# Optimization experiments

Measured on AMD Instinct MI355X. Metric: run time of the kernel, lower is better.

Reference implementation:

```python
import jax, jax.numpy as jnp
import numpy as np

N = 50000      # nodes
E = 800000     # edges (before self-loops)
D = 128        # input_dim
H = 128        # hidden_dim
G = 256        # graphs in batch


def setup_inputs() -> dict:
    key = jax.random.key(0)
    ks = jax.random.split(key, 6)
    x = jax.random.normal(ks[0], (N, D), dtype=jnp.float32)
    edge_index = jax.random.randint(ks[1], (2, E), 0, N, dtype=jnp.int32)
    batch = jnp.sort(jax.random.randint(ks[2], (N,), 0, G, dtype=jnp.int32))
    W1 = jax.random.normal(ks[3], (D, H), dtype=jnp.float32) / np.sqrt(D).astype(np.float32)
    b1 = jnp.zeros((H,), jnp.float32)
    W2 = jax.random.normal(ks[4], (H, H), dtype=jnp.float32) / np.sqrt(H).astype(np.float32)
    b2 = jnp.zeros((H,), jnp.float32)
    alpha = jnp.full((H,), 0.25, jnp.float32)  # PReLU(hidden_dim) init
    return dict(x=x, edge_index=edge_index, batch=batch,
                W1=W1, b1=b1, W2=W2, b2=b2, alpha=alpha)


def _gcn_layer(z, W, b, src, dst, norm):
    # GCNConv: z' = D^{-1/2}(A+I)D^{-1/2} (z W) + b
    zw = z @ W                                            # [N,H] dense GEMM
    agg = jnp.zeros_like(zw).at[dst].add(norm[:, None] * zw[src])  # scatter-add over edges
    return agg + b


def reference(x, edge_index, batch, W1, b1, W2, b2, alpha):
    loop = jnp.arange(N, dtype=edge_index.dtype)
    src = jnp.concatenate([edge_index[0], loop])          # add self-loops
    dst = jnp.concatenate([edge_index[1], loop])
    deg = jnp.zeros((N,), x.dtype).at[dst].add(jnp.float32(1.0))
    dinv = jnp.where(deg > 0, jax.lax.rsqrt(deg), 0.0)
    norm = dinv[src] * dinv[dst]                          # [E+N] edge weights

    zs = []
    z = x
    for (W, b) in ((W1, b1), (W2, b2)):
        z = _gcn_layer(z, W, b, src, dst, norm)
        z = jnp.where(z > 0, z, alpha * z)                # channel-wise PReLU (shared)
        zs.append(z)

    gs = [jax.ops.segment_sum(zi, batch, num_segments=G) for zi in zs]  # global_add_pool
    g = jnp.concatenate(gs, axis=1)                       # [G, num_layers*H]
    return z, g
```

## Files before the change

kernel.cpp:

```cpp
#include <hip/hip_runtime.h>
#include <stdint.h>


#define CAP 96

typedef __attribute__((ext_vector_type(8))) short short8;
typedef __attribute__((ext_vector_type(4))) float f32x4;

__device__ __forceinline__ uint16_t bf16rne(float f) {
    uint32_t u = __float_as_uint(f);
    uint32_t r = (u + 0x7fffu + ((u >> 16) & 1u)) >> 16;
    return (uint16_t)r;
}
__device__ __forceinline__ float bf_lo(uint32_t v) { return __uint_as_float(v << 16); }
__device__ __forceinline__ float bf_hi(uint32_t v) { return __uint_as_float(v & 0xffff0000u); }

__global__ __launch_bounds__(512) void k0(int* __restrict__ cursor, int nbC, int N,
                                          const float* __restrict__ W1,
                                          const float* __restrict__ W2,
                                          uint16_t* __restrict__ Wf1,
                                          uint16_t* __restrict__ Wf2,
                                          float* __restrict__ g_out, int nbZ) {
    int bid = blockIdx.x, t = threadIdx.x;
    if (bid < nbC) {
        int i = bid * 512 + t;
        if (i < N) cursor[i] = 0;
    } else if (bid < nbC + 8) {
        int tid = (bid - nbC) * 512 + t;
        const float* W = (tid & 2048) ? W2 : W1;
        uint16_t* O = (tid & 2048) ? Wf2 : Wf1;
        int q16 = tid & 2047;
        int lane = q16 & 63, n0ks = q16 >> 6;
        int n0 = n0ks >> 2, ks = n0ks & 3;
        int m = lane & 15, quad = lane >> 4;
        int nn = n0 * 16 + m;
        int kkb = ks * 32 + quad * 8;
        uint16_t v[8];
#pragma unroll
        for (int j = 0; j < 8; ++j) v[j] = bf16rne(W[(kkb + j) * 128 + nn]);
        *(short8*)&O[q16 * 8] = *(short8*)v;
    } else {
        int idx = (bid - nbC - 8) * 512 + t;
        ((float4*)g_out)[idx] = make_float4(0.f, 0.f, 0.f, 0.f);
    }
}

__device__ __forceinline__ void gemm_body(const float* Xf, const uint16_t* Xb,
                                          const uint16_t* __restrict__ Wf,
                                          uint16_t* __restrict__ Y, int nrows,
                                          uint16_t* Wl, int bid, int t) {
    int lane = t & 63, w = t >> 6;
    int row0 = bid * 128;
    for (int c = t; c < 2048; c += 512)
        *(short8*)&Wl[c * 8] = *(const short8*)&Wf[c * 8];
    int m = lane & 15, quad = lane >> 4;
    int arow = row0 + w * 16 + m;
    bool rowok = arow < nrows;
    short8 a[4];
    short8 zer = {0, 0, 0, 0, 0, 0, 0, 0};
    if (Xb) {
        const uint16_t* aptr = Xb + (size_t)arow * 128 + quad * 8;
#pragma unroll
        for (int ks = 0; ks < 4; ++ks)
            a[ks] = rowok ? *(const short8*)(aptr + ks * 32) : zer;
    } else {
        const float* ap = Xf + (size_t)arow * 128 + quad * 8;
#pragma unroll
        for (int ks = 0; ks < 4; ++ks) {
            if (rowok) {
                float4 u0 = *(const float4*)(ap + ks * 32);
                float4 u1 = *(const float4*)(ap + ks * 32 + 4);
                uint32_t q[4];
                q[0] = (uint32_t)bf16rne(u0.x) | ((uint32_t)bf16rne(u0.y) << 16);
                q[1] = (uint32_t)bf16rne(u0.z) | ((uint32_t)bf16rne(u0.w) << 16);
                q[2] = (uint32_t)bf16rne(u1.x) | ((uint32_t)bf16rne(u1.y) << 16);
                q[3] = (uint32_t)bf16rne(u1.z) | ((uint32_t)bf16rne(u1.w) << 16);
                a[ks] = *(short8*)q;
            } else a[ks] = zer;
        }
    }
    __syncthreads();

    f32x4 acc[8];
#pragma unroll
    for (int i = 0; i < 8; ++i) acc[i] = (f32x4){0.f, 0.f, 0.f, 0.f};
#pragma unroll
    for (int ks = 0; ks < 4; ++ks)
#pragma unroll
        for (int n0 = 0; n0 < 8; ++n0) {
            short8 b = *(short8*)&Wl[((n0 * 4 + ks) * 64 + lane) * 8];
            acc[n0] = __builtin_amdgcn_mfma_f32_16x16x32_bf16(a[ks], b, acc[n0], 0, 0, 0);
        }
    __syncthreads();

    uint16_t* Ep = Wl;
#pragma unroll
    for (int n0 = 0; n0 < 8; ++n0)
#pragma unroll
        for (int r = 0; r < 4; ++r)
            Ep[(w * 16 + quad * 4 + r) * 136 + n0 * 16 + m] = bf16rne(acc[n0][r]);
    for (int r16 = 0; r16 < 16; ++r16) {
        int row = row0 + w * 16 + r16;
        if (row < nrows) {
            uint32_t v = *(uint32_t*)&Ep[(w * 16 + r16) * 136 + lane * 2];
            ((uint32_t*)Y)[(size_t)row * 64 + lane] = v;
        }
    }
}

__device__ __forceinline__ void fill_body(const int* __restrict__ src, const int* __restrict__ dst,
                                          int* __restrict__ cursor, uint16_t* __restrict__ col,
                                          int E, int fb, int t) {
    int base = fb * 2048 + t;
    int d[4], s[4], p[4];
#pragma unroll
    for (int k = 0; k < 4; ++k) {
        int e = base + k * 512;
        d[k] = (e < E) ? dst[e] : -1;
        s[k] = (e < E) ? src[e] : 0;
    }
#pragma unroll
    for (int k = 0; k < 4; ++k) if (d[k] >= 0) p[k] = atomicAdd(&cursor[d[k]], 1);
#pragma unroll
    for (int k = 0; k < 4; ++k)
        if (d[k] >= 0 && p[k] < CAP) col[(size_t)d[k] * CAP + p[k]] = (uint16_t)s[k];
}

__global__ __launch_bounds__(512, 8) void k5(const float* __restrict__ X,
                                             const uint16_t* __restrict__ Wf,
                                             uint16_t* __restrict__ Y, int nrows, int gemmGrid,
                                             const int* __restrict__ src, const int* __restrict__ dst,
                                             int* __restrict__ cursor, uint16_t* __restrict__ col,
                                             int E, int fillGrid) {
    __shared__ uint16_t Wl[17408];
    int bid = blockIdx.x, t = threadIdx.x;
    int mn = min(gemmGrid, fillGrid), mn2 = 2 * mn;
    int role, idx;
    if (bid < mn2) { role = bid & 1; idx = bid >> 1; }
    else { role = (gemmGrid > fillGrid) ? 0 : 1; idx = bid - mn2 + mn; }
    if (role == 0) gemm_body(X, nullptr, Wf, Y, nrows, Wl, idx, t);
    else fill_body(src, dst, cursor, col, E, idx, t);
}

__global__ __launch_bounds__(512, 8) void gemm2k(const uint16_t* __restrict__ Xb,
                                                 const uint16_t* __restrict__ Wf,
                                                 uint16_t* __restrict__ Y, int nrows) {
    __shared__ uint16_t Wl[17408];
    gemm_body(nullptr, Xb, Wf, Y, nrows, Wl, blockIdx.x, threadIdx.x);
}

__global__ __launch_bounds__(256) void aggp(const uint32_t* __restrict__ zw,
                                            const int* __restrict__ cnt,
                                            const uint16_t* __restrict__ col,
                                            const float* __restrict__ bias,
                                            const float* __restrict__ alpha,
                                            const int* __restrict__ batch,
                                            float* __restrict__ gout, int col_off,
                                            uint32_t* __restrict__ z1b,
                                            float* __restrict__ zoutf,
                                            int mode, int n) {
    __shared__ int gsh[4];
    __shared__ float red[4][128];
    int wv = threadIdx.x >> 6;
    int lane = threadIdx.x & 63;
    int node = blockIdx.x * 4 + wv;
    bool valid = node < n;
    int nc = __builtin_amdgcn_readfirstlane(valid ? node : (n - 1));
    int c = lane * 2;
    int deg = cnt[nc];
    float di = rsqrtf((float)(deg + 1));
    uint32_t sv = zw[(size_t)nc * 64 + lane];
    float ax = di * bf_lo(sv), ay = di * bf_hi(sv);
    float bx = 0.f, by = 0.f;
    int len = min(deg, CAP);
    const uint32_t* cbu = (const uint32_t*)(col + (size_t)nc * CAP);
    uint32_t cc = cbu[lane < 48 ? lane : 0];
    int e = 0;
    for (; e + 7 < len; e += 8) {
        int h = e >> 1;
        uint32_t p0 = (uint32_t)__builtin_amdgcn_readlane((int)cc, h);
        uint32_t p1 = (uint32_t)__builtin_amdgcn_readlane((int)cc, h + 1);
        uint32_t p2 = (uint32_t)__builtin_amdgcn_readlane((int)cc, h + 2);
        uint32_t p3 = (uint32_t)__builtin_amdgcn_readlane((int)cc, h + 3);
        int s0 = (int)(p0 & 0xffffu), s1 = (int)(p0 >> 16);
        int s2 = (int)(p1 & 0xffffu), s3 = (int)(p1 >> 16);
        int s4 = (int)(p2 & 0xffffu), s5 = (int)(p2 >> 16);
        int s6 = (int)(p3 & 0xffffu), s7 = (int)(p3 >> 16);
        uint32_t v0 = zw[(size_t)s0 * 64 + lane];
        uint32_t v1 = zw[(size_t)s1 * 64 + lane];
        uint32_t v2 = zw[(size_t)s2 * 64 + lane];
        uint32_t v3 = zw[(size_t)s3 * 64 + lane];
        uint32_t v4 = zw[(size_t)s4 * 64 + lane];
        uint32_t v5 = zw[(size_t)s5 * 64 + lane];
        uint32_t v6 = zw[(size_t)s6 * 64 + lane];
        uint32_t v7 = zw[(size_t)s7 * 64 + lane];
        float w0 = rsqrtf((float)(cnt[s0] + 1));
        float w1 = rsqrtf((float)(cnt[s1] + 1));
        float w2 = rsqrtf((float)(cnt[s2] + 1));
        float w3 = rsqrtf((float)(cnt[s3] + 1));
        float w4 = rsqrtf((float)(cnt[s4] + 1));
        float w5 = rsqrtf((float)(cnt[s5] + 1));
        float w6 = rsqrtf((float)(cnt[s6] + 1));
        float w7 = rsqrtf((float)(cnt[s7] + 1));
        ax += w0 * bf_lo(v0); ay += w0 * bf_hi(v0);
        bx += w1 * bf_lo(v1); by += w1 * bf_hi(v1);
        ax += w2 * bf_lo(v2); ay += w2 * bf_hi(v2);
        bx += w3 * bf_lo(v3); by += w3 * bf_hi(v3);
        ax += w4 * bf_lo(v4); ay += w4 * bf_hi(v4);
        bx += w5 * bf_lo(v5); by += w5 * bf_hi(v5);
        ax += w6 * bf_lo(v6); ay += w6 * bf_hi(v6);
        bx += w7 * bf_lo(v7); by += w7 * bf_hi(v7);
    }
    for (; e < len; ++e) {
        uint32_t p = (uint32_t)__builtin_amdgcn_readlane((int)cc, e >> 1);
        int s = (e & 1) ? (int)(p >> 16) : (int)(p & 0xffffu);
        float w = rsqrtf((float)(cnt[s] + 1));
        uint32_t v = zw[(size_t)s * 64 + lane];
        ax += w * bf_lo(v); ay += w * bf_hi(v);
    }
    ax += bx; ay += by;
    float zx = di * ax + bias[c];
    float zy = di * ay + bias[c + 1];
    float px = alpha[c], py = alpha[c + 1];
    zx = zx > 0.f ? zx : px * zx;
    zy = zy > 0.f ? zy : py * zy;

    if (valid) {
        if (mode == 0) {
            uint32_t pk = (uint32_t)bf16rne(zx) | ((uint32_t)bf16rne(zy) << 16);
            z1b[(size_t)nc * 64 + lane] = pk;
        } else {
            ((float2*)zoutf)[(size_t)nc * 64 + lane] = make_float2(zx, zy);
        }
    }

    int g = batch[nc];
    float cx = valid ? zx : 0.f, cy = valid ? zy : 0.f;
    if (lane == 0) gsh[wv] = valid ? g : -1 - wv;
    __syncthreads();
    bool uni = (gsh[0] == gsh[1]) && (gsh[1] == gsh[2]) && (gsh[2] == gsh[3]);
    if (uni) {
        red[wv][c] = cx; red[wv][c + 1] = cy;
        __syncthreads();
        if (wv == 0) {
            float sx = red[0][c] + red[1][c] + red[2][c] + red[3][c];
            float sy = red[0][c + 1] + red[1][c + 1] + red[2][c + 1] + red[3][c + 1];
            float* base = &gout[(size_t)g * 256 + col_off];
            atomicAdd(&base[c], sx);
            atomicAdd(&base[c + 1], sy);
        }
    } else {
        __syncthreads();
        if (valid) {
            float* base = &gout[(size_t)g * 256 + col_off];
            atomicAdd(&base[c], cx);
            atomicAdd(&base[c + 1], cy);
        }
    }
}

extern "C" void kernel_launch(void* const* d_in, const int* in_sizes, int n_in,
                              void* d_out, int out_size, void* d_ws, size_t ws_size,
                              hipStream_t stream) {
    const float* x     = (const float*)d_in[0];
    const int*   eidx  = (const int*)d_in[1];
    const int*   batch = (const int*)d_in[2];
    const float* W1    = (const float*)d_in[3];
    const float* b1    = (const float*)d_in[4];
    const float* W2    = (const float*)d_in[5];
    const float* b2    = (const float*)d_in[6];
    const float* alpha = (const float*)d_in[7];

    const int N = in_sizes[2];
    const int E = in_sizes[1] / 2;
    const int G = (out_size - N * 128) / 256;

    const int* src = eidx;
    const int* dst = eidx + E;

    char* ws = (char*)d_ws;
    size_t off = 0;
    auto alloc = [&](size_t bytes) { void* q = ws + off; off = (off + bytes + 255) & ~(size_t)255; return q; };
    int*      cursor = (int*)alloc((size_t)N * 4);
    uint16_t* col    = (uint16_t*)alloc((size_t)N * CAP * 2);
    uint32_t* zw     = (uint32_t*)alloc((size_t)N * 128 * 2);
    uint32_t* z1b    = (uint32_t*)alloc((size_t)N * 128 * 2);
    uint16_t* Wf1    = (uint16_t*)alloc(128 * 128 * 2);
    uint16_t* Wf2    = (uint16_t*)alloc(128 * 128 * 2);

    float* z_out = (float*)d_out;
    float* g_out = (float*)d_out + (size_t)N * 128;

    int nbC      = (N + 511) / 512;
    int nbZ      = (G * 256 / 4 + 511) / 512;
    int fillGrid = (E + 2047) / 2048;
    int gemmGrid = (N + 127) / 128;
    int aggGrid  = (N + 3) / 4;

    k0<<<nbC + 8 + nbZ, 512, 0, stream>>>(cursor, nbC, N, W1, W2, Wf1, Wf2, g_out, nbZ);
    k5<<<gemmGrid + fillGrid, 512, 0, stream>>>(x, Wf1, (uint16_t*)zw, N, gemmGrid,
                                                src, dst, cursor, col, E, fillGrid);
    aggp<<<aggGrid, 256, 0, stream>>>(zw, cursor, col, b1, alpha, batch,
                                      g_out, 0, z1b, nullptr, 0, N);
    gemm2k<<<gemmGrid, 512, 0, stream>>>((const uint16_t*)z1b, Wf2, (uint16_t*)zw, N);
    aggp<<<aggGrid, 256, 0, stream>>>(zw, cursor, col, b2, alpha, batch,
                                      g_out, 128, nullptr, z_out, 1, N);
}
```

Measured before the change: 233.2 us.

## Pad neighbor gather with zero sentinel row, unroll by 16, resize gemm2 and fill blocks

The aggregation loop now walks neighbors 16 at a time. Padding slots point at an extra zeroed sentinel row (index N) with cnt=0, which removes the scalar tail loop and lets more independent gathers be in flight. The second GEMM is launched with 256-thread blocks of 64 rows for more blocks, and each fill block handles 4096 edges instead of 2048. The cost is extra sentinel loads on padded slots, higher register pressure in aggp, and one extra row in the cursor and zw buffers.

Measured after the change: 244.9 us. +5.0%, slower.

```diff
diff --git a/kernel.cpp b/kernel.cpp
--- a/kernel.cpp
+++ b/kernel.cpp
@@ -20,11 +20,13 @@
                                           const float* __restrict__ W2,
                                           uint16_t* __restrict__ Wf1,
                                           uint16_t* __restrict__ Wf2,
-                                          float* __restrict__ g_out, int nbZ) {
+                                          float* __restrict__ g_out, int nbZ,
+                                          uint32_t* __restrict__ zw) {
     int bid = blockIdx.x, t = threadIdx.x;
     if (bid < nbC) {
         int i = bid * 512 + t;
-        if (i < N) cursor[i] = 0;
+        if (i <= N) cursor[i] = 0;
+        if (bid == 0 && t < 64) zw[(size_t)N * 64 + t] = 0u;
     } else if (bid < nbC + 8) {
         int tid = (bid - nbC) * 512 + t;
         const float* W = (tid & 2048) ? W2 : W1;
@@ -45,13 +47,14 @@
     }
 }
 
+template <int NW>
 __device__ __forceinline__ void gemm_body(const float* Xf, const uint16_t* Xb,
                                           const uint16_t* __restrict__ Wf,
                                           uint16_t* __restrict__ Y, int nrows,
                                           uint16_t* Wl, int bid, int t) {
     int lane = t & 63, w = t >> 6;
-    int row0 = bid * 128;
-    for (int c = t; c < 2048; c += 512)
+    int row0 = bid * (NW * 16);
+    for (int c = t; c < 2048; c += NW * 64)
         *(short8*)&Wl[c * 8] = *(const short8*)&Wf[c * 8];
     int m = lane & 15, quad = lane >> 4;
     int arow = row0 + w * 16 + m;
@@ -111,18 +114,18 @@
 __device__ __forceinline__ void fill_body(const int* __restrict__ src, const int* __restrict__ dst,
                                           int* __restrict__ cursor, uint16_t* __restrict__ col,
                                           int E, int fb, int t) {
-    int base = fb * 2048 + t;
-    int d[4], s[4], p[4];
-#pragma unroll
-    for (int k = 0; k < 4; ++k) {
+    int base = fb * 4096 + t;
+    int d[8], s[8], p[8];
+#pragma unroll
+    for (int k = 0; k < 8; ++k) {
         int e = base + k * 512;
         d[k] = (e < E) ? dst[e] : -1;
         s[k] = (e < E) ? src[e] : 0;
     }
 #pragma unroll
-    for (int k = 0; k < 4; ++k) if (d[k] >= 0) p[k] = atomicAdd(&cursor[d[k]], 1);
-#pragma unroll
-    for (int k = 0; k < 4; ++k)
+    for (int k = 0; k < 8; ++k) if (d[k] >= 0) p[k] = atomicAdd(&cursor[d[k]], 1);
+#pragma unroll
+    for (int k = 0; k < 8; ++k)
         if (d[k] >= 0 && p[k] < CAP) col[(size_t)d[k] * CAP + p[k]] = (uint16_t)s[k];
 }
 
@@ -138,15 +141,15 @@
     int role, idx;
     if (bid < mn2) { role = bid & 1; idx = bid >> 1; }
     else { role = (gemmGrid > fillGrid) ? 0 : 1; idx = bid - mn2 + mn; }
-    if (role == 0) gemm_body(X, nullptr, Wf, Y, nrows, Wl, idx, t);
+    if (role == 0) gemm_body<8>(X, nullptr, Wf, Y, nrows, Wl, idx, t);
     else fill_body(src, dst, cursor, col, E, idx, t);
 }
 
-__global__ __launch_bounds__(512, 8) void gemm2k(const uint16_t* __restrict__ Xb,
+__global__ __launch_bounds__(256, 4) void gemm2k(const uint16_t* __restrict__ Xb,
                                                  const uint16_t* __restrict__ Wf,
                                                  uint16_t* __restrict__ Y, int nrows) {
     __shared__ uint16_t Wl[17408];
-    gemm_body(nullptr, Xb, Wf, Y, nrows, Wl, blockIdx.x, threadIdx.x);
+    gemm_body<4>(nullptr, Xb, Wf, Y, nrows, Wl, blockIdx.x, threadIdx.x);
 }
 
 __global__ __launch_bounds__(256) void aggp(const uint32_t* __restrict__ zw,
@@ -173,19 +176,99 @@
     float ax = di * bf_lo(sv), ay = di * bf_hi(sv);
     float bx = 0.f, by = 0.f;
     int len = min(deg, CAP);
+    int len8 = (len + 7) & ~7;
     const uint32_t* cbu = (const uint32_t*)(col + (size_t)nc * CAP);
     uint32_t cc = cbu[lane < 48 ? lane : 0];
     int e = 0;
-    for (; e + 7 < len; e += 8) {
+    for (; e + 16 <= len8; e += 16) {
         int h = e >> 1;
-        uint32_t p0 = (uint32_t)__builtin_amdgcn_readlane((int)cc, h);
-        uint32_t p1 = (uint32_t)__builtin_amdgcn_readlane((int)cc, h + 1);
-        uint32_t p2 = (uint32_t)__builtin_amdgcn_readlane((int)cc, h + 2);
-        uint32_t p3 = (uint32_t)__builtin_amdgcn_readlane((int)cc, h + 3);
-        int s0 = (int)(p0 & 0xffffu), s1 = (int)(p0 >> 16);
-        int s2 = (int)(p1 & 0xffffu), s3 = (int)(p1 >> 16);
-        int s4 = (int)(p2 & 0xffffu), s5 = (int)(p2 >> 16);
-        int s6 = (int)(p3 & 0xffffu), s7 = (int)(p3 >> 16);
+        uint32_t q0 = (uint32_t)__builtin_amdgcn_readlane((int)cc, h);
+        uint32_t q1 = (uint32_t)__builtin_amdgcn_readlane((int)cc, h + 1);
+        uint32_t q2 = (uint32_t)__builtin_amdgcn_readlane((int)cc, h + 2);
+        uint32_t q3 = (uint32_t)__builtin_amdgcn_readlane((int)cc, h + 3);
+        uint32_t q4 = (uint32_t)__builtin_amdgcn_readlane((int)cc, h + 4);
+        uint32_t q5 = (uint32_t)__builtin_amdgcn_readlane((int)cc, h + 5);
+        uint32_t q6 = (uint32_t)__builtin_amdgcn_readlane((int)cc, h + 6);
+        uint32_t q7 = (uint32_t)__builtin_amdgcn_readlane((int)cc, h + 7);
+        int s0  = (e +  0 < len) ? (int)(q0 & 0xffffu) : n;
+        int s1  = (e +  1 < len) ? (int)(q0 >> 16)     : n;
+        int s2  = (e +  2 < len) ? (int)(q1 & 0xffffu) : n;
+        int s3  = (e +  3 < len) ? (int)(q1 >> 16)     : n;
+        int s4  = (e +  4 < len) ? (int)(q2 & 0xffffu) : n;
+        int s5  = (e +  5 < len) ? (int)(q2 >> 16)     : n;
+        int s6  = (e +  6 < len) ? (int)(q3 & 0xffffu) : n;
+        int s7  = (e +  7 < len) ? (int)(q3 >> 16)     : n;
+        int s8  = (e +  8 < len) ? (int)(q4 & 0xffffu) : n;
+        int s9  = (e +  9 < len) ? (int)(q4 >> 16)     : n;
+        int s10 = (e + 10 < len) ? (int)(q5 & 0xffffu) : n;
+        int s11 = (e + 11 < len) ? (int)(q5 >> 16)     : n;
+        int s12 = (e + 12 < len) ? (int)(q6 & 0xffffu) : n;
+        int s13 = (e + 13 < len) ? (int)(q6 >> 16)     : n;
+        int s14 = (e + 14 < len) ? (int)(q7 & 0xffffu) : n;
+        int s15 = (e + 15 < len) ? (int)(q7 >> 16)     : n;
+        uint32_t v0  = zw[(size_t)s0  * 64 + lane];
+        uint32_t v1  = zw[(size_t)s1  * 64 + lane];
+        uint32_t v2  = zw[(size_t)s2  * 64 + lane];
+        uint32_t v3  = zw[(size_t)s3  * 64 + lane];
+        uint32_t v4  = zw[(size_t)s4  * 64 + lane];
+        uint32_t v5  = zw[(size_t)s5  * 64 + lane];
+        uint32_t v6  = zw[(size_t)s6  * 64 + lane];
+        uint32_t v7  = zw[(size_t)s7  * 64 + lane];
+        uint32_t v8  = zw[(size_t)s8  * 64 + lane];
+        uint32_t v9  = zw[(size_t)s9  * 64 + lane];
+        uint32_t v10 = zw[(size_t)s10 * 64 + lane];
+        uint32_t v11 = zw[(size_t)s11 * 64 + lane];
+        uint32_t v12 = zw[(size_t)s12 * 64 + lane];
+        uint32_t v13 = zw[(size_t)s13 * 64 + lane];
+        uint32_t v14 = zw[(size_t)s14 * 64 + lane];
+        uint32_t v15 = zw[(size_t)s15 * 64 + lane];
+        float w0  = rsqrtf((float)(cnt[s0]  + 1));
+        float w1  = rsqrtf((float)(cnt[s1]  + 1));
+        float w2  = rsqrtf((float)(cnt[s2]  + 1));
+        float w3  = rsqrtf((float)(cnt[s3]  + 1));
+        float w4  = rsqrtf((float)(cnt[s4]  + 1));
+        float w5  = rsqrtf((float)(cnt[s5]  + 1));
+        float w6  = rsqrtf((float)(cnt[s6]  + 1));
+        float w7  = rsqrtf((float)(cnt[s7]  + 1));
+        float w8  = rsqrtf((float)(cnt[s8]  + 1));
+        float w9  = rsqrtf((float)(cnt[s9]  + 1));
+        float w10 = rsqrtf((float)(cnt[s10] + 1));
+        float w11 = rsqrtf((float)(cnt[s11] + 1));
+        float w12 = rsqrtf((float)(cnt[s12] + 1));
+        float w13 = rsqrtf((float)(cnt[s13] + 1));
+        float w14 = rsqrtf((float)(cnt[s14] + 1));
+        float w15 = rsqrtf((float)(cnt[s15] + 1));
+        ax += w0  * bf_lo(v0);  ay += w0  * bf_hi(v0);
+        bx += w1  * bf_lo(v1);  by += w1  * bf_hi(v1);
+        ax += w2  * bf_lo(v2);  ay += w2  * bf_hi(v2);
+        bx += w3  * bf_lo(v3);  by += w3  * bf_hi(v3);
+        ax += w4  * bf_lo(v4);  ay += w4  * bf_hi(v4);
+        bx += w5  * bf_lo(v5);  by += w5  * bf_hi(v5);
+        ax += w6  * bf_lo(v6);  ay += w6  * bf_hi(v6);
+        bx += w7  * bf_lo(v7);  by += w7  * bf_hi(v7);
+        ax += w8  * bf_lo(v8);  ay += w8  * bf_hi(v8);
+        bx += w9  * bf_lo(v9);  by += w9  * bf_hi(v9);
+        ax += w10 * bf_lo(v10); ay += w10 * bf_hi(v10);
+        bx += w11 * bf_lo(v11); by += w11 * bf_hi(v11);
+        ax += w12 * bf_lo(v12); ay += w12 * bf_hi(v12);
+        bx += w13 * bf_lo(v13); by += w13 * bf_hi(v13);
+        ax += w14 * bf_lo(v14); ay += w14 * bf_hi(v14);
+        bx += w15 * bf_lo(v15); by += w15 * bf_hi(v15);
+    }
+    if (e < len8) {
+        int h = e >> 1;
+        uint32_t q0 = (uint32_t)__builtin_amdgcn_readlane((int)cc, h);
+        uint32_t q1 = (uint32_t)__builtin_amdgcn_readlane((int)cc, h + 1);
+        uint32_t q2 = (uint32_t)__builtin_amdgcn_readlane((int)cc, h + 2);
+        uint32_t q3 = (uint32_t)__builtin_amdgcn_readlane((int)cc, h + 3);
+        int s0 = (e + 0 < len) ? (int)(q0 & 0xffffu) : n;
+        int s1 = (e + 1 < len) ? (int)(q0 >> 16)     : n;
+        int s2 = (e + 2 < len) ? (int)(q1 & 0xffffu) : n;
+        int s3 = (e + 3 < len) ? (int)(q1 >> 16)     : n;
+        int s4 = (e + 4 < len) ? (int)(q2 & 0xffffu) : n;
+        int s5 = (e + 5 < len) ? (int)(q2 >> 16)     : n;
+        int s6 = (e + 6 < len) ? (int)(q3 & 0xffffu) : n;
+        int s7 = (e + 7 < len) ? (int)(q3 >> 16)     : n;
         uint32_t v0 = zw[(size_t)s0 * 64 + lane];
         uint32_t v1 = zw[(size_t)s1 * 64 + lane];
         uint32_t v2 = zw[(size_t)s2 * 64 + lane];
@@ -211,13 +294,6 @@
         ax += w6 * bf_lo(v6); ay += w6 * bf_hi(v6);
         bx += w7 * bf_lo(v7); by += w7 * bf_hi(v7);
     }
-    for (; e < len; ++e) {
-        uint32_t p = (uint32_t)__builtin_amdgcn_readlane((int)cc, e >> 1);
-        int s = (e & 1) ? (int)(p >> 16) : (int)(p & 0xffffu);
-        float w = rsqrtf((float)(cnt[s] + 1));
-        uint32_t v = zw[(size_t)s * 64 + lane];
-        ax += w * bf_lo(v); ay += w * bf_hi(v);
-    }
     ax += bx; ay += by;
     float zx = di * ax + bias[c];
     float zy = di * ay + bias[c + 1];
@@ -281,9 +357,9 @@
     char* ws = (char*)d_ws;
     size_t off = 0;
     auto alloc = [&](size_t bytes) { void* q = ws + off; off = (off + bytes + 255) & ~(size_t)255; return q; };
-    int*      cursor = (int*)alloc((size_t)N * 4);
+    int*      cursor = (int*)alloc((size_t)(N + 1) * 4);
     uint16_t* col    = (uint16_t*)alloc((size_t)N * CAP * 2);
-    uint32_t* zw     = (uint32_t*)alloc((size_t)N * 128 * 2);
+    uint32_t* zw     = (uint32_t*)alloc((size_t)(N + 1) * 128 * 2);
     uint32_t* z1b    = (uint32_t*)alloc((size_t)N * 128 * 2);
     uint16_t* Wf1    = (uint16_t*)alloc(128 * 128 * 2);
     uint16_t* Wf2    = (uint16_t*)alloc(128 * 128 * 2);
@@ -291,18 +367,19 @@
     float* z_out = (float*)d_out;
     float* g_out = (float*)d_out + (size_t)N * 128;
 
-    int nbC      = (N + 511) / 512;
+    int nbC      = (N + 512) / 512;
     int nbZ      = (G * 256 / 4 + 511) / 512;
-    int fillGrid = (E + 2047) / 2048;
+    int fillGrid = (E + 4095) / 4096;
     int gemmGrid = (N + 127) / 128;
+    int gemm2Grid = (N + 63) / 64;
     int aggGrid  = (N + 3) / 4;
 
-    k0<<<nbC + 8 + nbZ, 512, 0, stream>>>(cursor, nbC, N, W1, W2, Wf1, Wf2, g_out, nbZ);
+    k0<<<nbC + 8 + nbZ, 512, 0, stream>>>(cursor, nbC, N, W1, W2, Wf1, Wf2, g_out, nbZ, zw);
     k5<<<gemmGrid + fillGrid, 512, 0, stream>>>(x, Wf1, (uint16_t*)zw, N, gemmGrid,
                                                 src, dst, cursor, col, E, fillGrid);
     aggp<<<aggGrid, 256, 0, stream>>>(zw, cursor, col, b1, alpha, batch,
                                       g_out, 0, z1b, nullptr, 0, N);
-    gemm2k<<<gemmGrid, 512, 0, stream>>>((const uint16_t*)z1b, Wf2, (uint16_t*)zw, N);
+    gemm2k<<<gemm2Grid, 256, 0, stream>>>((const uint16_t*)z1b, Wf2, (uint16_t*)zw, N);
     aggp<<<aggGrid, 256, 0, stream>>>(zw, cursor, col, b2, alpha, batch,
                                       g_out, 128, nullptr, z_out, 1, N);
 }
```

## Prescale layer-2 GEMM rows by source degree norm and pad gathers to 16-wide

Applied to the files above, without the earlier changes.

The second GEMM now multiplies each output row by rsqrt(deg+1), so the layer-2 aggregation no longer has to gather cnt[s] and compute rsqrt per edge. The aggregation loop is also restructured to issue 16 independent gathers per iteration. Out-of-range slots are padded to a dummy zero row at index N, which removes the scalar tail loop. This adds an extra zero row to zw and cursor. It also applies bf16 rounding after the degree scaling in layer 2, which changes numerics slightly.

Result: faster. 228.3 us (-2.1%).

```diff
diff --git a/kernel.cpp b/kernel.cpp
--- a/kernel.cpp
+++ b/kernel.cpp
@@ -20,11 +20,13 @@
                                           const float* __restrict__ W2,
                                           uint16_t* __restrict__ Wf1,
                                           uint16_t* __restrict__ Wf2,
-                                          float* __restrict__ g_out, int nbZ) {
+                                          float* __restrict__ g_out, int nbZ,
+                                          uint32_t* __restrict__ zw) {
     int bid = blockIdx.x, t = threadIdx.x;
     if (bid < nbC) {
         int i = bid * 512 + t;
-        if (i < N) cursor[i] = 0;
+        if (i <= N) cursor[i] = 0;
+        if (bid == 0 && t < 64) zw[(size_t)N * 64 + t] = 0u;
     } else if (bid < nbC + 8) {
         int tid = (bid - nbC) * 512 + t;
         const float* W = (tid & 2048) ? W2 : W1;
@@ -48,6 +50,7 @@
 __device__ __forceinline__ void gemm_body(const float* Xf, const uint16_t* Xb,
                                           const uint16_t* __restrict__ Wf,
                                           uint16_t* __restrict__ Y, int nrows,
+                                          const int* __restrict__ cnt,
                                           uint16_t* Wl, int bid, int t) {
     int lane = t & 63, w = t >> 6;
     int row0 = bid * 128;
@@ -93,12 +96,22 @@
         }
     __syncthreads();
 
+    float dsc[4] = {1.f, 1.f, 1.f, 1.f};
+    if (cnt) {
+#pragma unroll
+        for (int r = 0; r < 4; ++r) {
+            int gr = row0 + w * 16 + quad * 4 + r;
+            int d = (gr < nrows) ? cnt[gr] : 0;
+            dsc[r] = rsqrtf((float)(d + 1));
+        }
+    }
+
     uint16_t* Ep = Wl;
 #pragma unroll
     for (int n0 = 0; n0 < 8; ++n0)
 #pragma unroll
         for (int r = 0; r < 4; ++r)
-            Ep[(w * 16 + quad * 4 + r) * 136 + n0 * 16 + m] = bf16rne(acc[n0][r]);
+            Ep[(w * 16 + quad * 4 + r) * 136 + n0 * 16 + m] = bf16rne(acc[n0][r] * dsc[r]);
     for (int r16 = 0; r16 < 16; ++r16) {
         int row = row0 + w * 16 + r16;
         if (row < nrows) {
@@ -138,17 +151,19 @@
     int role, idx;
     if (bid < mn2) { role = bid & 1; idx = bid >> 1; }
     else { role = (gemmGrid > fillGrid) ? 0 : 1; idx = bid - mn2 + mn; }
-    if (role == 0) gemm_body(X, nullptr, Wf, Y, nrows, Wl, idx, t);
+    if (role == 0) gemm_body(X, nullptr, Wf, Y, nrows, nullptr, Wl, idx, t);
     else fill_body(src, dst, cursor, col, E, idx, t);
 }
 
 __global__ __launch_bounds__(512, 8) void gemm2k(const uint16_t* __restrict__ Xb,
                                                  const uint16_t* __restrict__ Wf,
-                                                 uint16_t* __restrict__ Y, int nrows) {
+                                                 uint16_t* __restrict__ Y, int nrows,
+                                                 const int* __restrict__ cnt) {
     __shared__ uint16_t Wl[17408];
-    gemm_body(nullptr, Xb, Wf, Y, nrows, Wl, blockIdx.x, threadIdx.x);
-}
-
+    gemm_body(nullptr, Xb, Wf, Y, nrows, cnt, Wl, blockIdx.x, threadIdx.x);
+}
+
+template <bool PS>
 __global__ __launch_bounds__(256) void aggp(const uint32_t* __restrict__ zw,
                                             const int* __restrict__ cnt,
                                             const uint16_t* __restrict__ col,
@@ -170,53 +185,55 @@
     int deg = cnt[nc];
     float di = rsqrtf((float)(deg + 1));
     uint32_t sv = zw[(size_t)nc * 64 + lane];
-    float ax = di * bf_lo(sv), ay = di * bf_hi(sv);
+    float sw = PS ? 1.f : di;
+    float ax = sw * bf_lo(sv), ay = sw * bf_hi(sv);
     float bx = 0.f, by = 0.f;
     int len = min(deg, CAP);
+    int len8 = (len + 7) & ~7;
     const uint32_t* cbu = (const uint32_t*)(col + (size_t)nc * CAP);
     uint32_t cc = cbu[lane < 48 ? lane : 0];
     int e = 0;
-    for (; e + 7 < len; e += 8) {
+    for (; e + 16 <= len8; e += 16) {
         int h = e >> 1;
-        uint32_t p0 = (uint32_t)__builtin_amdgcn_readlane((int)cc, h);
-        uint32_t p1 = (uint32_t)__builtin_amdgcn_readlane((int)cc, h + 1);
-        uint32_t p2 = (uint32_t)__builtin_amdgcn_readlane((int)cc, h + 2);
-        uint32_t p3 = (uint32_t)__builtin_amdgcn_readlane((int)cc, h + 3);
-        int s0 = (int)(p0 & 0xffffu), s1 = (int)(p0 >> 16);
-        int s2 = (int)(p1 & 0xffffu), s3 = (int)(p1 >> 16);
-        int s4 = (int)(p2 & 0xffffu), s5 = (int)(p2 >> 16);
-        int s6 = (int)(p3 & 0xffffu), s7 = (int)(p3 >> 16);
-        uint32_t v0 = zw[(size_t)s0 * 64 + lane];
-        uint32_t v1 = zw[(size_t)s1 * 64 + lane];
-        uint32_t v2 = zw[(size_t)s2 * 64 + lane];
-        uint32_t v3 = zw[(size_t)s3 * 64 + lane];
-        uint32_t v4 = zw[(size_t)s4 * 64 + lane];
-        uint32_t v5 = zw[(size_t)s5 * 64 + lane];
-        uint32_t v6 = zw[(size_t)s6 * 64 + lane];
-        uint32_t v7 = zw[(size_t)s7 * 64 + lane];
-        float w0 = rsqrtf((float)(cnt[s0] + 1));
-        float w1 = rsqrtf((float)(cnt[s1] + 1));
-        float w2 = rsqrtf((float)(cnt[s2] + 1));
-        float w3 = rsqrtf((float)(cnt[s3] + 1));
-        float w4 = rsqrtf((float)(cnt[s4] + 1));
-        float w5 = rsqrtf((float)(cnt[s5] + 1));
-        float w6 = rsqrtf((float)(cnt[s6] + 1));
-        float w7 = rsqrtf((float)(cnt[s7] + 1));
-        ax += w0 * bf_lo(v0); ay += w0 * bf_hi(v0);
-        bx += w1 * bf_lo(v1); by += w1 * bf_hi(v1);
-        ax += w2 * bf_lo(v2); ay += w2 * bf_hi(v2);
-        bx += w3 * bf_lo(v3); by += w3 * bf_hi(v3);
-        ax += w4 * bf_lo(v4); ay += w4 * bf_hi(v4);
-        bx += w5 * bf_lo(v5); by += w5 * bf_hi(v5);
-        ax += w6 * bf_lo(v6); ay += w6 * bf_hi(v6);
-        bx += w7 * bf_lo(v7); by += w7 * bf_hi(v7);
-    }
-    for (; e < len; ++e) {
-        uint32_t p = (uint32_t)__builtin_amdgcn_readlane((int)cc, e >> 1);
-        int s = (e & 1) ? (int)(p >> 16) : (int)(p & 0xffffu);
-        float w = rsqrtf((float)(cnt[s] + 1));
-        uint32_t v = zw[(size_t)s * 64 + lane];
-        ax += w * bf_lo(v); ay += w * bf_hi(v);
+        int s[16];
+#pragma unroll
+        for (int j = 0; j < 8; ++j) {
+            uint32_t q = (uint32_t)__builtin_amdgcn_readlane((int)cc, h + j);
+            s[2 * j]     = (e + 2 * j     < len) ? (int)(q & 0xffffu) : n;
+            s[2 * j + 1] = (e + 2 * j + 1 < len) ? (int)(q >> 16)     : n;
+        }
+        uint32_t v[16];
+#pragma unroll
+        for (int j = 0; j < 16; ++j) v[j] = zw[(size_t)s[j] * 64 + lane];
+        float wg[16];
+#pragma unroll
+        for (int j = 0; j < 16; ++j) wg[j] = PS ? 1.f : rsqrtf((float)(cnt[s[j]] + 1));
+#pragma unroll
+        for (int j = 0; j < 16; ++j) {
+            if (j & 1) { bx += wg[j] * bf_lo(v[j]); by += wg[j] * bf_hi(v[j]); }
+            else       { ax += wg[j] * bf_lo(v[j]); ay += wg[j] * bf_hi(v[j]); }
+        }
+    }
+    if (e < len8) {
+        int h = e >> 1;
+        int s[8];
+#pragma unroll
+        for (int j = 0; j < 4; ++j) {
+            uint32_t q = (uint32_t)__builtin_amdgcn_readlane((int)cc, h + j);
+            s[2 * j]     = (e + 2 * j     < len) ? (int)(q & 0xffffu) : n;
+            s[2 * j + 1] = (e + 2 * j + 1 < len) ? (int)(q >> 16)     : n;
+        }
+        uint32_t v[8];
+#pragma unroll
+        for (int j = 0; j < 8; ++j) v[j] = zw[(size_t)s[j] * 64 + lane];
+        float wg[8];
+#pragma unroll
+        for (int j = 0; j < 8; ++j) wg[j] = PS ? 1.f : rsqrtf((float)(cnt[s[j]] + 1));
+#pragma unroll
+        for (int j = 0; j < 8; ++j) {
+            if (j & 1) { bx += wg[j] * bf_lo(v[j]); by += wg[j] * bf_hi(v[j]); }
+            else       { ax += wg[j] * bf_lo(v[j]); ay += wg[j] * bf_hi(v[j]); }
+        }
     }
     ax += bx; ay += by;
     float zx = di * ax + bias[c];
@@ -281,9 +298,9 @@
     char* ws = (char*)d_ws;
     size_t off = 0;
     auto alloc = [&](size_t bytes) { void* q = ws + off; off = (off + bytes + 255) & ~(size_t)255; return q; };
-    int*      cursor = (int*)alloc((size_t)N * 4);
+    int*      cursor = (int*)alloc((size_t)(N + 1) * 4);
     uint16_t* col    = (uint16_t*)alloc((size_t)N * CAP * 2);
-    uint32_t* zw     = (uint32_t*)alloc((size_t)N * 128 * 2);
+    uint32_t* zw     = (uint32_t*)alloc((size_t)(N + 1) * 128 * 2);
     uint32_t* z1b    = (uint32_t*)alloc((size_t)N * 128 * 2);
     uint16_t* Wf1    = (uint16_t*)alloc(128 * 128 * 2);
     uint16_t* Wf2    = (uint16_t*)alloc(128 * 128 * 2);
@@ -291,18 +308,18 @@
     float* z_out = (float*)d_out;
     float* g_out = (float*)d_out + (size_t)N * 128;
 
-    int nbC      = (N + 511) / 512;
+    int nbC      = (N + 512) / 512;
     int nbZ      = (G * 256 / 4 + 511) / 512;
     int fillGrid = (E + 2047) / 2048;
     int gemmGrid = (N + 127) / 128;
     int aggGrid  = (N + 3) / 4;
 
-    k0<<<nbC + 8 + nbZ, 512, 0, stream>>>(cursor, nbC, N, W1, W2, Wf1, Wf2, g_out, nbZ);
+    k0<<<nbC + 8 + nbZ, 512, 0, stream>>>(cursor, nbC, N, W1, W2, Wf1, Wf2, g_out, nbZ, zw);
     k5<<<gemmGrid + fillGrid, 512, 0, stream>>>(x, Wf1, (uint16_t*)zw, N, gemmGrid,
                                                 src, dst, cursor, col, E, fillGrid);
-    aggp<<<aggGrid, 256, 0, stream>>>(zw, cursor, col, b1, alpha, batch,
-                                      g_out, 0, z1b, nullptr, 0, N);
-    gemm2k<<<gemmGrid, 512, 0, stream>>>((const uint16_t*)z1b, Wf2, (uint16_t*)zw, N);
-    aggp<<<aggGrid, 256, 0, stream>>>(zw, cursor, col, b2, alpha, batch,
-                                      g_out, 128, nullptr, z_out, 1, N);
-}
+    aggp<false><<<aggGrid, 256, 0, stream>>>(zw, cursor, col, b1, alpha, batch,
+                                             g_out, 0, z1b, nullptr, 0, N);
+    gemm2k<<<gemmGrid, 512, 0, stream>>>((const uint16_t*)z1b, Wf2, (uint16_t*)zw, N, cursor);
+    aggp<true><<<aggGrid, 256, 0, stream>>>(zw, cursor, col, b2, alpha, batch,
+                                            g_out, 128, nullptr, z_out, 1, N);
+}
```
